# Performance work log

Measured on AMD Instinct MI355X. Metric: run time of the kernel, lower is better.

Reference implementation:

```python
import jax, jax.numpy as jnp
import numpy as np

DF, DK, DG, NR = 1024, 64, 64, 16
DV = DF // NR  # 64
N = 1024       # num_rois


def setup_inputs() -> dict:
    key = jax.random.key(0)
    ks = jax.random.split(key, 12)
    def xavier(k, out_d, in_d):
        lim = float(np.sqrt(6.0 / (in_d + out_d)))
        return jax.random.uniform(k, (out_d, in_d), jnp.float32, -lim, lim)
    return {
        "x": jax.random.normal(ks[0], (N, DF), jnp.float32),
        "position_embedding": jax.random.uniform(ks[1], (N, N, DG), jnp.float32),
        "Wq": xavier(ks[2], DK * NR, DF), "bq": jnp.zeros((DK * NR,), jnp.float32),
        "Wk": xavier(ks[3], DK * NR, DF), "bk": jnp.zeros((DK * NR,), jnp.float32),
        "Wv": xavier(ks[4], DF, DF),     "bv": jnp.zeros((DF,), jnp.float32),
        "Wg": xavier(ks[5], NR, DG),     "bg": jnp.zeros((NR,), jnp.float32),
        "Wy": xavier(ks[6], DF, DF),     "by": jnp.zeros((DF,), jnp.float32),
    }


def reference(x, position_embedding, Wq, bq, Wk, bk, Wv, bv, Wg, bg, Wy, by):
    n = x.shape[0]
    # geometry bias: linear -> relu -> clamp_min(1e-6) -> log, then head-major
    g = jnp.einsum('ijd,hd->hij', position_embedding, Wg) + bg[:, None, None]  # [Nr, N, N]
    g = jnp.log(jnp.maximum(jax.nn.relu(g), 1e-6))
    # projections, reshaped to [Nr, N, d]
    Q = (x @ Wq.T + bq).reshape(n, NR, DK).transpose(1, 0, 2)   # [Nr, N, dk]
    K = (x @ Wk.T + bk).reshape(n, NR, DK).transpose(1, 0, 2)   # [Nr, N, dk]
    V = (x @ Wv.T + bv).reshape(n, NR, DV).transpose(1, 0, 2)   # [Nr, N, dv]
    scores = jnp.einsum('hnd,hmd->hnm', Q, K) + g               # no 1/sqrt(dk) scaling (faithful)
    attn = jax.nn.softmax(scores, axis=2)
    Y = jnp.einsum('hnm,hmd->hnd', attn, V)                      # [Nr, N, dv]
    Y = Y.transpose(1, 0, 2).reshape(n, DF)
    y = Y @ Wy.T + by
    return x + y
```

## Files before the change

kernel.cpp:

```cpp
#include <hip/hip_runtime.h>
#include <hip/hip_bf16.h>


typedef __bf16 bf16_t;
typedef _Float16 f16_t;
typedef __attribute__((ext_vector_type(8))) __bf16 bf16x8;
typedef __attribute__((ext_vector_type(8))) _Float16 f16x8;
typedef __attribute__((ext_vector_type(4))) float f32x4;

__device__ inline bf16_t f2b(float f) {
    unsigned u = __builtin_bit_cast(unsigned, f);
    unsigned r = u + 0x7fffu + ((u >> 16) & 1u);
    unsigned short h = (unsigned short)(r >> 16);
    return __builtin_bit_cast(bf16_t, h);
}

__global__ __launch_bounds__(256) void fused_g_proj_k(
        const float* __restrict__ pe, const float* __restrict__ Wg, const float* __restrict__ bg,
        f16_t* __restrict__ Wout,
        const float* __restrict__ x,
        const float* __restrict__ Wq, const float* __restrict__ bq, bf16_t* __restrict__ Qb,
        const float* __restrict__ Wk, const float* __restrict__ bk, bf16_t* __restrict__ Kb,
        const float* __restrict__ Wv, const float* __restrict__ bv, bf16_t* __restrict__ Vb) {
    __shared__ bf16_t As[2][64][40];
    __shared__ bf16_t Bs[2][64][40];
    const int bid = blockIdx.x;
    const int t = threadIdx.x;

    if (bid < 768) {
        const int z = bid >> 8, rem = bid & 255;
        const float* B = (z == 0) ? Wq : (z == 1) ? Wk : Wv;
        const float* bias = (z == 0) ? bq : (z == 1) ? bk : bv;
        bf16_t* outp = (z == 0) ? Qb : (z == 1) ? Kb : Vb;
        const int m0 = (rem >> 4) * 64, n0 = (rem & 15) * 64;
        const int lr = t >> 2, lq = t & 3;

        auto stage = [&](bf16_t (*dst)[64][40], const float* __restrict__ Sp, int row0, int buf, int k0) {
            const float* p = Sp + (long)(row0 + lr) * 1024 + k0 + lq * 8;
            float4 u0 = *(const float4*)p;
            float4 u1 = *(const float4*)(p + 4);
            bf16x8 v;
            v[0] = f2b(u0.x); v[1] = f2b(u0.y); v[2] = f2b(u0.z); v[3] = f2b(u0.w);
            v[4] = f2b(u1.x); v[5] = f2b(u1.y); v[6] = f2b(u1.z); v[7] = f2b(u1.w);
            *(bf16x8*)&dst[buf][lr][lq * 8] = v;
        };

        const int wid = t >> 6, lane = t & 63;
        const int wm = (wid >> 1) * 32, wn = (wid & 1) * 32;
        const int ml = lane & 15, kl = (lane >> 4) * 8;
        f32x4 acc[2][2] = {};

        stage(As, x, m0, 0, 0);
        stage(Bs, B, n0, 0, 0);
        __syncthreads();
        for (int kt = 0; kt < 32; kt++) {
            const int buf = kt & 1;
            if (kt + 1 < 32) { stage(As, x, m0, buf ^ 1, (kt + 1) * 32); stage(Bs, B, n0, buf ^ 1, (kt + 1) * 32); }
            bf16x8 a0 = *(const bf16x8*)&As[buf][wm + ml][kl];
            bf16x8 a1 = *(const bf16x8*)&As[buf][wm + 16 + ml][kl];
            bf16x8 b0 = *(const bf16x8*)&Bs[buf][wn + ml][kl];
            bf16x8 b1 = *(const bf16x8*)&Bs[buf][wn + 16 + ml][kl];
            acc[0][0] = __builtin_amdgcn_mfma_f32_16x16x32_bf16(a0, b0, acc[0][0], 0, 0, 0);
            acc[0][1] = __builtin_amdgcn_mfma_f32_16x16x32_bf16(a0, b1, acc[0][1], 0, 0, 0);
            acc[1][0] = __builtin_amdgcn_mfma_f32_16x16x32_bf16(a1, b0, acc[1][0], 0, 0, 0);
            acc[1][1] = __builtin_amdgcn_mfma_f32_16x16x32_bf16(a1, b1, acc[1][1], 0, 0, 0);
            __syncthreads();
        }

#pragma unroll
        for (int mt = 0; mt < 2; mt++)
#pragma unroll
            for (int nt = 0; nt < 2; nt++) {
                f32x4 v = acc[mt][nt];
                const int rbase = m0 + wm + mt * 16 + ((lane >> 4) << 2);
                const int col = n0 + wn + nt * 16 + (lane & 15);
#pragma unroll
                for (int r = 0; r < 4; r++) {
                    const int row = rbase + r;
                    float val = v[r] + bias[col];
                    int h = col >> 6, d = col & 63;
                    if (z < 2) outp[((long)h << 16) + ((long)row << 6) + d] = f2b(val);
                    else       outp[((long)h << 16) + ((long)d << 10) + row] = f2b(val);
                }
            }
    } else {
        const long row = (long)(bid - 768) * 256 + t;
        const float4* pr = (const float4*)(pe + (row << 6));

        float p[16];
        float4 pv[8];
#pragma unroll
        for (int q = 0; q < 8; q++) pv[q] = pr[q];
#pragma unroll
        for (int h = 0; h < 16; h++) {
            const float4* wg4 = (const float4*)(Wg + (h << 6));
            float a = 0.f;
#pragma unroll
            for (int q = 0; q < 8; q++) {
                float4 w = wg4[q];
                a += pv[q].x * w.x + pv[q].y * w.y + pv[q].z * w.z + pv[q].w * w.w;
            }
            p[h] = a;
        }
#pragma unroll
        for (int q = 0; q < 8; q++) pv[q] = pr[8 + q];
#pragma unroll
        for (int h = 0; h < 16; h++) {
            const float4* wg4 = (const float4*)(Wg + (h << 6) + 32);
            float a = p[h];
#pragma unroll
            for (int q = 0; q < 8; q++) {
                float4 w = wg4[q];
                a += pv[q].x * w.x + pv[q].y * w.y + pv[q].z * w.z + pv[q].w * w.w;
            }
            a += bg[h];
            Wout[((long)h << 20) + row] = (f16_t)fmaxf(a, 1e-6f);
        }
    }
}

__global__ __launch_bounds__(256) void gemmY_k(const bf16_t* __restrict__ A,
                                               const float* __restrict__ Bw,
                                               const float* __restrict__ bias,
                                               float* __restrict__ outp,
                                               const float* __restrict__ extra) {
    __shared__ bf16_t As[2][64][40];
    __shared__ bf16_t Bs[2][64][40];
    const int t = threadIdx.x;
    const int m0 = blockIdx.y * 64, n0 = blockIdx.x * 64;
    const int lr = t >> 2, lq = t & 3;

    auto stageA = [&](int buf, int k0) {
        const bf16_t* p = A + (long)(m0 + lr) * 1024 + k0 + lq * 8;
        *(bf16x8*)&As[buf][lr][lq * 8] = *(const bf16x8*)p;
    };
    auto stageB = [&](int buf, int k0) {
        const float* p = Bw + (long)(n0 + lr) * 1024 + k0 + lq * 8;
        float4 u0 = *(const float4*)p;
        float4 u1 = *(const float4*)(p + 4);
        bf16x8 v;
        v[0] = f2b(u0.x); v[1] = f2b(u0.y); v[2] = f2b(u0.z); v[3] = f2b(u0.w);
        v[4] = f2b(u1.x); v[5] = f2b(u1.y); v[6] = f2b(u1.z); v[7] = f2b(u1.w);
        *(bf16x8*)&Bs[buf][lr][lq * 8] = v;
    };

    const int wid = t >> 6, lane = t & 63;
    const int wm = (wid >> 1) * 32, wn = (wid & 1) * 32;
    const int ml = lane & 15, kl = (lane >> 4) * 8;
    f32x4 acc[2][2] = {};

    stageA(0, 0);
    stageB(0, 0);
    __syncthreads();
    for (int kt = 0; kt < 32; kt++) {
        const int buf = kt & 1;
        if (kt + 1 < 32) { stageA(buf ^ 1, (kt + 1) * 32); stageB(buf ^ 1, (kt + 1) * 32); }
        bf16x8 a0 = *(const bf16x8*)&As[buf][wm + ml][kl];
        bf16x8 a1 = *(const bf16x8*)&As[buf][wm + 16 + ml][kl];
        bf16x8 b0 = *(const bf16x8*)&Bs[buf][wn + ml][kl];
        bf16x8 b1 = *(const bf16x8*)&Bs[buf][wn + 16 + ml][kl];
        acc[0][0] = __builtin_amdgcn_mfma_f32_16x16x32_bf16(a0, b0, acc[0][0], 0, 0, 0);
        acc[0][1] = __builtin_amdgcn_mfma_f32_16x16x32_bf16(a0, b1, acc[0][1], 0, 0, 0);
        acc[1][0] = __builtin_amdgcn_mfma_f32_16x16x32_bf16(a1, b0, acc[1][0], 0, 0, 0);
        acc[1][1] = __builtin_amdgcn_mfma_f32_16x16x32_bf16(a1, b1, acc[1][1], 0, 0, 0);
        __syncthreads();
    }

#pragma unroll
    for (int mt = 0; mt < 2; mt++)
#pragma unroll
        for (int nt = 0; nt < 2; nt++) {
            f32x4 v = acc[mt][nt];
            const int rbase = m0 + wm + mt * 16 + ((lane >> 4) << 2);
            const int col = n0 + wn + nt * 16 + (lane & 15);
#pragma unroll
            for (int r = 0; r < 4; r++) {
                const int row = rbase + r;
                long idx = ((long)row << 10) + col;
                outp[idx] = v[r] + bias[col] + extra[idx];
            }
        }
}

__global__ __launch_bounds__(256) void attn_kernel(const bf16_t* __restrict__ Q,
                                                   const bf16_t* __restrict__ K,
                                                   const bf16_t* __restrict__ Vt,
                                                   const f16_t* __restrict__ Wf,
                                                   bf16_t* __restrict__ Y) {
    __shared__ bf16_t Qs[64][72];
    __shared__ bf16_t Ks[2][64][72];
    __shared__ bf16_t Vts[2][64][72];
    __shared__ f16_t  Ws[2][64][72];
    __shared__ bf16_t Ps[4][16][72];

    const int qt = blockIdx.x, h = blockIdx.y;
    const int t = threadIdx.x;
    const int w = t >> 6, lane = t & 63;
    const int ml = lane & 15, kq = lane >> 4;
    const int q0 = qt << 6;
    const int sr = t >> 2, sc = (t & 3) << 4;

    const bf16_t* Kh = K + ((long)h << 16);
    const bf16_t* Vh = Vt + ((long)h << 16);
    const f16_t*  Wh = Wf + ((long)h << 20) + ((long)(q0 + sr) << 10);

    {
        const bf16_t* src = Q + ((long)h << 16) + ((long)(q0 + sr) << 6) + sc;
        *(bf16x8*)&Qs[sr][sc]     = *(const bf16x8*)src;
        *(bf16x8*)&Qs[sr][sc + 8] = *(const bf16x8*)(src + 8);
        const bf16_t* ks = Kh + ((long)sr << 6) + sc;
        *(bf16x8*)&Ks[0][sr][sc]     = *(const bf16x8*)ks;
        *(bf16x8*)&Ks[0][sr][sc + 8] = *(const bf16x8*)(ks + 8);
        const bf16_t* vs = Vh + ((long)sr << 10) + sc;
        *(bf16x8*)&Vts[0][sr][sc]     = *(const bf16x8*)vs;
        *(bf16x8*)&Vts[0][sr][sc + 8] = *(const bf16x8*)(vs + 8);
        const f16_t* gs = Wh + sc;
        *(f16x8*)&Ws[0][sr][sc]     = *(const f16x8*)gs;
        *(f16x8*)&Ws[0][sr][sc + 8] = *(const f16x8*)(gs + 8);
    }
    __syncthreads();

    const bf16x8 aq0 = *(const bf16x8*)&Qs[(w << 4) + ml][kq * 8];
    const bf16x8 aq1 = *(const bf16x8*)&Qs[(w << 4) + ml][32 + kq * 8];

    f32x4 O[4] = {};
    float lsum[4] = {0.f, 0.f, 0.f, 0.f};

    int buf = 0;
    for (int kt = 0; kt < 16; kt++) {
        bf16x8 rk0, rk1, rv0, rv1;
        f16x8 rw0, rw1;
        const bool pf = (kt < 15);
        if (pf) {
            const int k0 = (kt + 1) << 6;
            const bf16_t* ks = Kh + ((long)(k0 + sr) << 6) + sc;
            rk0 = *(const bf16x8*)ks; rk1 = *(const bf16x8*)(ks + 8);
            const bf16_t* vs = Vh + ((long)sr << 10) + k0 + sc;
            rv0 = *(const bf16x8*)vs; rv1 = *(const bf16x8*)(vs + 8);
            const f16_t* gs = Wh + k0 + sc;
            rw0 = *(const f16x8*)gs; rw1 = *(const f16x8*)(gs + 8);
        }

        f32x4 s[4] = {};
#pragma unroll
        for (int c = 0; c < 4; c++) {
            bf16x8 bk0 = *(const bf16x8*)&Ks[buf][(c << 4) + ml][kq * 8];
            bf16x8 bk1 = *(const bf16x8*)&Ks[buf][(c << 4) + ml][32 + kq * 8];
            s[c] = __builtin_amdgcn_mfma_f32_16x16x32_bf16(aq0, bk0, s[c], 0, 0, 0);
            s[c] = __builtin_amdgcn_mfma_f32_16x16x32_bf16(aq1, bk1, s[c], 0, 0, 0);
        }
#pragma unroll
        for (int c = 0; c < 4; c++) {
#pragma unroll
            for (int r = 0; r < 4; r++) {
                float wv = (float)Ws[buf][(w << 4) + (kq << 2) + r][(c << 4) + ml];
                float p = __expf(s[c][r]) * wv;
                lsum[r] += p;
                Ps[w][(kq << 2) + r][(c << 4) + ml] = f2b(p);
            }
        }
        const bf16x8 pa0 = *(const bf16x8*)&Ps[w][ml][kq * 8];
        const bf16x8 pa1 = *(const bf16x8*)&Ps[w][ml][32 + kq * 8];
#pragma unroll
        for (int c = 0; c < 4; c++) {
            bf16x8 v0 = *(const bf16x8*)&Vts[buf][(c << 4) + ml][kq * 8];
            bf16x8 v1 = *(const bf16x8*)&Vts[buf][(c << 4) + ml][32 + kq * 8];
            O[c] = __builtin_amdgcn_mfma_f32_16x16x32_bf16(pa0, v0, O[c], 0, 0, 0);
            O[c] = __builtin_amdgcn_mfma_f32_16x16x32_bf16(pa1, v1, O[c], 0, 0, 0);
        }

        if (pf) {
            const int nb = buf ^ 1;
            *(bf16x8*)&Ks[nb][sr][sc]      = rk0;
            *(bf16x8*)&Ks[nb][sr][sc + 8]  = rk1;
            *(bf16x8*)&Vts[nb][sr][sc]     = rv0;
            *(bf16x8*)&Vts[nb][sr][sc + 8] = rv1;
            *(f16x8*)&Ws[nb][sr][sc]       = rw0;
            *(f16x8*)&Ws[nb][sr][sc + 8]   = rw1;
        }
        __syncthreads();
        buf ^= 1;
    }

#pragma unroll
    for (int r = 0; r < 4; r++) {
        float v = lsum[r];
        v += __shfl_xor(v, 1); v += __shfl_xor(v, 2);
        v += __shfl_xor(v, 4); v += __shfl_xor(v, 8);
        lsum[r] = 1.0f / v;
    }
    const int rowb = q0 + (w << 4) + (kq << 2);
    const int colb = (h << 6) + ml;
#pragma unroll
    for (int c = 0; c < 4; c++)
#pragma unroll
        for (int r = 0; r < 4; r++)
            Y[((long)(rowb + r) << 10) + colb + (c << 4)] = f2b(O[c][r] * lsum[r]);
}

extern "C" void kernel_launch(void* const* d_in, const int* in_sizes, int n_in,
                              void* d_out, int out_size, void* d_ws, size_t ws_size,
                              hipStream_t stream) {
    const float* x  = (const float*)d_in[0];
    const float* pe = (const float*)d_in[1];
    const float* Wq = (const float*)d_in[2];
    const float* bq = (const float*)d_in[3];
    const float* Wk = (const float*)d_in[4];
    const float* bk = (const float*)d_in[5];
    const float* Wv = (const float*)d_in[6];
    const float* bv = (const float*)d_in[7];
    const float* Wg = (const float*)d_in[8];
    const float* bg = (const float*)d_in[9];
    const float* Wy = (const float*)d_in[10];
    const float* by = (const float*)d_in[11];

    char* ws = (char*)d_ws;
    f16_t*  Wf = (f16_t*)ws;
    bf16_t* Qb = (bf16_t*)(ws + (32ul << 20));
    bf16_t* Kb = (bf16_t*)(ws + (34ul << 20));
    bf16_t* Vb = (bf16_t*)(ws + (36ul << 20));
    bf16_t* Yb = (bf16_t*)(ws + (38ul << 20));

    fused_g_proj_k<<<768 + 4096, 256, 0, stream>>>(pe, Wg, bg, Wf,
                                                   x, Wq, bq, Qb, Wk, bk, Kb, Wv, bv, Vb);
    attn_kernel<<<dim3(16, 16), 256, 0, stream>>>(Qb, Kb, Vb, Wf, Yb);
    gemmY_k<<<dim3(16, 16), 256, 0, stream>>>(Yb, Wy, by, (float*)d_out, x);
}
```

Measured before the change: 142.6 us.

## Coalesce position-embedding loads with lane-split dot products and LDS transpose

Rewrites the geometry-bias path so four lanes share each position-embedding row, loading interleaved float4 chunks that coalesce across the wave. Partial dot products are combined with xor shuffles, each lane keeps four of the sixteen heads, and results are staged in shared memory so the head-major f16 output is written contiguously. Loads for the next group of rows are prefetched during compute, the geometry blocks are placed ahead of the projection GEMM blocks in the grid, and a launch-bounds occupancy hint is added. This targets the strided per-thread 256-byte row reads of the old path, at the cost of extra shuffles and LDS traffic.

```diff
diff --git a/kernel.cpp b/kernel.cpp
--- a/kernel.cpp
+++ b/kernel.cpp
@@ -6,7 +6,9 @@
 typedef _Float16 f16_t;
 typedef __attribute__((ext_vector_type(8))) __bf16 bf16x8;
 typedef __attribute__((ext_vector_type(8))) _Float16 f16x8;
+typedef __attribute__((ext_vector_type(2))) _Float16 f16x2;
 typedef __attribute__((ext_vector_type(4))) float f32x4;
+typedef __attribute__((ext_vector_type(2))) float f32x2;
 
 __device__ inline bf16_t f2b(float f) {
     unsigned u = __builtin_bit_cast(unsigned, f);
@@ -15,24 +17,90 @@
     return __builtin_bit_cast(bf16_t, h);
 }
 
-__global__ __launch_bounds__(256) void fused_g_proj_k(
+__global__ __launch_bounds__(256, 6) void fused_g_proj_k(
         const float* __restrict__ pe, const float* __restrict__ Wg, const float* __restrict__ bg,
         f16_t* __restrict__ Wout,
         const float* __restrict__ x,
         const float* __restrict__ Wq, const float* __restrict__ bq, bf16_t* __restrict__ Qb,
         const float* __restrict__ Wk, const float* __restrict__ bk, bf16_t* __restrict__ Kb,
         const float* __restrict__ Wv, const float* __restrict__ bv, bf16_t* __restrict__ Vb) {
-    __shared__ bf16_t As[2][64][40];
-    __shared__ bf16_t Bs[2][64][40];
+    __shared__ char smem_raw[20480];
     const int bid = blockIdx.x;
     const int t = threadIdx.x;
 
-    if (bid < 768) {
-        const int z = bid >> 8, rem = bid & 255;
+    if (bid < 4096) {
+        const int w = t >> 6, lane = t & 63;
+        const int r = lane >> 2, c = lane & 3;
+        const long g0 = ((long)bid * 4 + w) * 64;
+        f16_t* gout = (f16_t*)smem_raw + w * (64 * 18);
+
+        const float* pebase = pe + (g0 << 6);
+        float4 pc0, pc1, pc2, pc3, pn0, pn1, pn2, pn3;
+        {
+            const float* p0 = pebase + (r << 6) + (c << 2);
+            pc0 = *(const float4*)(p0);
+            pc1 = *(const float4*)(p0 + 16);
+            pc2 = *(const float4*)(p0 + 32);
+            pc3 = *(const float4*)(p0 + 48);
+        }
+        unsigned cof = c << 2;
+        for (int s = 0; s < 4; s++) {
+            if (s < 3) {
+                const float* p1 = pebase + (((s + 1) * 16 + r) << 6) + (c << 2);
+                pn0 = *(const float4*)(p1);
+                pn1 = *(const float4*)(p1 + 16);
+                pn2 = *(const float4*)(p1 + 32);
+                pn3 = *(const float4*)(p1 + 48);
+            }
+            asm volatile("" : "+v"(cof));
+            float p[16];
+#pragma unroll
+            for (int h = 0; h < 16; h++) {
+                const float* wgh = Wg + (h << 6) + cof;
+                float4 w0 = *(const float4*)(wgh);
+                float4 w1 = *(const float4*)(wgh + 16);
+                float4 w2 = *(const float4*)(wgh + 32);
+                float4 w3 = *(const float4*)(wgh + 48);
+                f32x2 a = {0.f, 0.f};
+                a = __builtin_elementwise_fma((f32x2){pc0.x, pc0.y}, (f32x2){w0.x, w0.y}, a);
+                a = __builtin_elementwise_fma((f32x2){pc0.z, pc0.w}, (f32x2){w0.z, w0.w}, a);
+                a = __builtin_elementwise_fma((f32x2){pc1.x, pc1.y}, (f32x2){w1.x, w1.y}, a);
+                a = __builtin_elementwise_fma((f32x2){pc1.z, pc1.w}, (f32x2){w1.z, w1.w}, a);
+                a = __builtin_elementwise_fma((f32x2){pc2.x, pc2.y}, (f32x2){w2.x, w2.y}, a);
+                a = __builtin_elementwise_fma((f32x2){pc2.z, pc2.w}, (f32x2){w2.z, w2.w}, a);
+                a = __builtin_elementwise_fma((f32x2){pc3.x, pc3.y}, (f32x2){w3.x, w3.y}, a);
+                a = __builtin_elementwise_fma((f32x2){pc3.z, pc3.w}, (f32x2){w3.z, w3.w}, a);
+                p[h] = a.x + a.y;
+            }
+#pragma unroll
+            for (int h = 0; h < 16; h++) {
+                p[h] += __shfl_xor(p[h], 1);
+                p[h] += __shfl_xor(p[h], 2);
+                p[h] = fmaxf(p[h] + bg[h], 1e-6f);
+            }
+            float s0 = (c & 2) ? ((c & 1) ? p[12] : p[8]) : ((c & 1) ? p[4] : p[0]);
+            float s1 = (c & 2) ? ((c & 1) ? p[13] : p[9]) : ((c & 1) ? p[5] : p[1]);
+            float s2 = (c & 2) ? ((c & 1) ? p[14] : p[10]) : ((c & 1) ? p[6] : p[2]);
+            float s3 = (c & 2) ? ((c & 1) ? p[15] : p[11]) : ((c & 1) ? p[7] : p[3]);
+            const int ob = (s * 16 + r) * 18 + (c << 2);
+            *(f16x2*)&gout[ob]     = (f16x2){(f16_t)s0, (f16_t)s1};
+            *(f16x2*)&gout[ob + 2] = (f16x2){(f16_t)s2, (f16_t)s3};
+            if (s < 3) { pc0 = pn0; pc1 = pn1; pc2 = pn2; pc3 = pn3; }
+        }
+#pragma unroll
+        for (int h = 0; h < 16; h++) {
+            f16_t v = gout[lane * 18 + h];
+            Wout[((long)h << 20) + g0 + lane] = v;
+        }
+    } else {
+        bf16_t (*As)[64][40] = (bf16_t(*)[64][40])smem_raw;
+        bf16_t (*Bs)[64][40] = (bf16_t(*)[64][40])(smem_raw + 10240);
+        const int rem = bid - 4096;
+        const int z = rem >> 8, rem2 = rem & 255;
         const float* B = (z == 0) ? Wq : (z == 1) ? Wk : Wv;
         const float* bias = (z == 0) ? bq : (z == 1) ? bk : bv;
         bf16_t* outp = (z == 0) ? Qb : (z == 1) ? Kb : Vb;
-        const int m0 = (rem >> 4) * 64, n0 = (rem & 15) * 64;
+        const int m0 = (rem2 >> 4) * 64, n0 = (rem2 & 15) * 64;
         const int lr = t >> 2, lq = t & 3;
 
         auto stage = [&](bf16_t (*dst)[64][40], const float* __restrict__ Sp, int row0, int buf, int k0) {
@@ -83,39 +151,6 @@
                     else       outp[((long)h << 16) + ((long)d << 10) + row] = f2b(val);
                 }
             }
-    } else {
-        const long row = (long)(bid - 768) * 256 + t;
-        const float4* pr = (const float4*)(pe + (row << 6));
-
-        float p[16];
-        float4 pv[8];
-#pragma unroll
-        for (int q = 0; q < 8; q++) pv[q] = pr[q];
-#pragma unroll
-        for (int h = 0; h < 16; h++) {
-            const float4* wg4 = (const float4*)(Wg + (h << 6));
-            float a = 0.f;
-#pragma unroll
-            for (int q = 0; q < 8; q++) {
-                float4 w = wg4[q];
-                a += pv[q].x * w.x + pv[q].y * w.y + pv[q].z * w.z + pv[q].w * w.w;
-            }
-            p[h] = a;
-        }
-#pragma unroll
-        for (int q = 0; q < 8; q++) pv[q] = pr[8 + q];
-#pragma unroll
-        for (int h = 0; h < 16; h++) {
-            const float4* wg4 = (const float4*)(Wg + (h << 6) + 32);
-            float a = p[h];
-#pragma unroll
-            for (int q = 0; q < 8; q++) {
-                float4 w = wg4[q];
-                a += pv[q].x * w.x + pv[q].y * w.y + pv[q].z * w.z + pv[q].w * w.w;
-            }
-            a += bg[h];
-            Wout[((long)h << 20) + row] = (f16_t)fmaxf(a, 1e-6f);
-        }
     }
 }
 
@@ -321,7 +356,7 @@
     bf16_t* Vb = (bf16_t*)(ws + (36ul << 20));
     bf16_t* Yb = (bf16_t*)(ws + (38ul << 20));
 
-    fused_g_proj_k<<<768 + 4096, 256, 0, stream>>>(pe, Wg, bg, Wf,
+    fused_g_proj_k<<<4096 + 768, 256, 0, stream>>>(pe, Wg, bg, Wf,
                                                    x, Wq, bq, Qb, Wk, bk, Kb, Wv, bv, Vb);
     attn_kernel<<<dim3(16, 16), 256, 0, stream>>>(Qb, Kb, Vb, Wf, Yb);
     gemmY_k<<<dim3(16, 16), 256, 0, stream>>>(Yb, Wy, by, (float*)d_out, x);
```

Measured after the change: 253.4 us. 77.7% more time.
